# Kernel optimization log

Measured on AMD Instinct MI355X. Metric: run time of the kernel, lower is better.

Reference implementation:

```python
import jax, jax.numpy as jnp
import numpy as np

B, N, C, H = 4, 2048, 768, 12


def setup_inputs() -> dict:
    key = jax.random.key(0)
    k1, k2, k3 = jax.random.split(key, 3)
    x = jax.random.normal(k1, (B, N, C), dtype=jnp.float32)
    qkv_w = jax.random.normal(k2, (3 * C, C), dtype=jnp.float32) * 0.02
    proj_w = jax.random.normal(k3, (C, C), dtype=jnp.float32) * 0.02
    proj_b = jnp.zeros((C,), dtype=jnp.float32)
    return {"x": x, "qkv_w": qkv_w, "proj_w": proj_w, "proj_b": proj_b}


def reference(x, qkv_w, proj_w, proj_b):
    b, n, c = x.shape
    hd = c // H
    scale = hd ** -0.5
    # qkv projection (no bias): (B,N,3C) -> (3,B,H,N,hd)
    qkv = (x @ qkv_w.T).reshape(b, n, 3, H, hd).transpose(2, 0, 3, 1, 4)
    q = qkv[0] * scale
    k = qkv[1]
    v = qkv[2]
    attn = jax.nn.softmax(jnp.einsum('bhqd,bhkd->bhqk', q, k), axis=-1)
    out = jnp.einsum('bhqk,bhkd->bhqd', attn, v)  # (B,H,N,hd)
    out = out.transpose(0, 2, 1, 3).reshape(b, n, c)
    return out @ proj_w.T + proj_b
```

## Files before the change

kernel.cpp:

```cpp
#include <hip/hip_runtime.h>

#define B_SZ 4
#define SEQ  2048
#define CH   768
#define NH   12
#define HD   64

typedef float f32x4  __attribute__((ext_vector_type(4)));
typedef __bf16 bf16x8 __attribute__((ext_vector_type(8)));
typedef __bf16 bf16x2 __attribute__((ext_vector_type(2)));

#define MFMA16(a,b,c) __builtin_amdgcn_mfma_f32_16x16x32_bf16(a,b,c,0,0,0)

#define QSCALE 0.1803368801111204f

#if __has_builtin(__builtin_amdgcn_exp2f)
#define EXP2(x) __builtin_amdgcn_exp2f(x)
#else
#define EXP2(x) exp2f(x)
#endif

#define SWZ(row) (((row) ^ ((row) >> 3)) & 7)

__device__ __forceinline__ unsigned pack2(float a, float b) {
    union { bf16x2 v; unsigned u; } p;
    p.v[0] = (__bf16)a; p.v[1] = (__bf16)b;
    return p.u;
}

__device__ __forceinline__ void lds_dma16(const void* g, void* l) {
    __builtin_amdgcn_global_load_lds(
        (const __attribute__((address_space(1))) void*)g,
        (__attribute__((address_space(3))) void*)(unsigned)(unsigned long long)l,
        16, 0, 0);
}

#define NBLK_X  6144
#define NBLK_W  1728
#define NBLK_P   576
__global__ __launch_bounds__(256) void convert_all(const float* __restrict__ x,
                                                   const float* __restrict__ w,
                                                   const float* __restrict__ p,
                                                   __bf16* __restrict__ ox,
                                                   __bf16* __restrict__ ow,
                                                   __bf16* __restrict__ op) {
    int blk = blockIdx.x;
    const float* src;
    __bf16* dst;
    int base;
    if (blk < NBLK_X)               { src = x; dst = ox; base = blk; }
    else if (blk < NBLK_X + NBLK_W) { src = w; dst = ow; base = blk - NBLK_X; }
    else                            { src = p; dst = op; base = blk - NBLK_X - NBLK_W; }
    int i = (base * 256 + threadIdx.x) * 4;
    float4 v = *(const float4*)(src + i);
    union { __bf16 h[4]; uint2 u; } o;
    o.h[0] = (__bf16)v.x; o.h[1] = (__bf16)v.y; o.h[2] = (__bf16)v.z; o.h[3] = (__bf16)v.w;
    *(uint2*)(dst + i) = o.u;
}

__device__ __forceinline__ void gemm128_loop(const __bf16* __restrict__ A,
                                             const __bf16* __restrict__ Bm,
                                             int K, int rowBlk, int colBlk,
                                             __bf16* As, __bf16* Bs,
                                             f32x4 acc[4][4]) {
    const int tid  = threadIdx.x;
    const int lane = tid & 63, wid = tid >> 6;
    const int quad = lane >> 4, l16 = lane & 15;
    const int wm = wid >> 1, wn = wid & 1;

    f32x4 z = {0.f, 0.f, 0.f, 0.f};
#pragma unroll
    for (int mi = 0; mi < 4; ++mi)
#pragma unroll
        for (int ni = 0; ni < 4; ++ni) acc[mi][ni] = z;

    for (int k0 = 0; k0 < K; k0 += 64) {
        __syncthreads();
#pragma unroll
        for (int i = 0; i < 4; ++i) {
            int s = i * 256 + tid;
            int row = s >> 3, pc = s & 7;
            int lc = pc ^ (row & 7);
            lds_dma16(A  + (size_t)(rowBlk + row) * K + k0 + lc * 8, As + s * 8);
            lds_dma16(Bm + (size_t)(colBlk + row) * K + k0 + lc * 8, Bs + s * 8);
        }
        __syncthreads();

#pragma unroll
        for (int kc = 0; kc < 2; ++kc) {
            bf16x8 af[4], bfr[4];
#pragma unroll
            for (int mi = 0; mi < 4; ++mi) {
                int row = wm * 64 + mi * 16 + l16;
                int pc = (quad + 4 * kc) ^ (row & 7);
                af[mi] = *(const bf16x8*)(As + row * 64 + pc * 8);
            }
#pragma unroll
            for (int ni = 0; ni < 4; ++ni) {
                int row = wn * 64 + ni * 16 + l16;
                int pc = (quad + 4 * kc) ^ (row & 7);
                bfr[ni] = *(const bf16x8*)(Bs + row * 64 + pc * 8);
            }
#pragma unroll
            for (int mi = 0; mi < 4; ++mi)
#pragma unroll
                for (int ni = 0; ni < 4; ++ni)
                    acc[mi][ni] = MFMA16(af[mi], bfr[ni], acc[mi][ni]);
        }
    }
}

__global__ __launch_bounds__(256) void qkv_gemm(const __bf16* __restrict__ Xb,
                                                const __bf16* __restrict__ Wb,
                                                __bf16* __restrict__ Qb,
                                                __bf16* __restrict__ Kb,
                                                __bf16* __restrict__ Vt) {
    __shared__ __bf16 smem[128 * 128];
    f32x4 acc[4][4];
    const int rowBlk = blockIdx.x * 128, colBlk = blockIdx.y * 128;
    gemm128_loop(Xb, Wb, CH, rowBlk, colBlk, smem, smem + 128 * 64, acc);

    const int tid = threadIdx.x;
    const int lane = tid & 63, wid = tid >> 6;
    const int quad = lane >> 4, l16 = lane & 15, wm = wid >> 1, wn = wid & 1;
    const int b = rowBlk >> 11, n0 = rowBlk & (SEQ - 1);

    if (colBlk < 2 * CH) {
        const int isK = (colBlk >= CH);
#pragma unroll
        for (int mi = 0; mi < 4; ++mi)
#pragma unroll
            for (int ni = 0; ni < 4; ++ni)
#pragma unroll
                for (int r = 0; r < 4; ++r) {
                    int n = n0 + wm * 64 + mi * 16 + quad * 4 + r;
                    int cc = colBlk - (isK ? CH : 0) + wn * 64 + ni * 16 + l16;
                    int h = cc >> 6, d = cc & 63;
                    size_t idx = (size_t)((b * NH + h) * SEQ + n) * HD + d;
                    float v = acc[mi][ni][r];
                    if (isK) Kb[idx] = (__bf16)v;
                    else     Qb[idx] = (__bf16)(v * QSCALE);
                }
    } else {
        const int vblk = colBlk - 2 * CH;
        __syncthreads();
#pragma unroll
        for (int mi = 0; mi < 4; ++mi)
#pragma unroll
            for (int ni = 0; ni < 4; ++ni)
#pragma unroll
                for (int r = 0; r < 4; ++r) {
                    int rl = wm * 64 + mi * 16 + quad * 4 + r;
                    int cl = wn * 64 + ni * 16 + l16;
                    smem[cl * 128 + (((rl >> 3) ^ (cl & 15)) << 3) + (rl & 7)] =
                        (__bf16)acc[mi][ni][r];
                }
        __syncthreads();
        const int dl = tid >> 1;
        const int d  = vblk + dl;
        const int h  = d >> 6, dd = d & 63;
        const size_t base = (size_t)((b * NH + h) * HD + dd) * SEQ + n0;
#pragma unroll
        for (int j2 = 0; j2 < 8; ++j2) {
            int j = (tid & 1) * 8 + j2;
            uint4 val = *(const uint4*)(smem + dl * 128 + ((j ^ (dl & 15)) << 3));
            *(uint4*)(Vt + base + j * 8) = val;
        }
    }
}

__global__ __launch_bounds__(256, 3) void flash_attn(const __bf16* __restrict__ Qb,
                                                     const __bf16* __restrict__ Kb,
                                                     const __bf16* __restrict__ Vt,
                                                     __bf16* __restrict__ Ab) {
    __shared__ __bf16 smem[16384];

    const int tid  = threadIdx.x;
    const int lane = tid & 63, wid = tid >> 6;
    const int quad = lane >> 4, l16 = lane & 15;

    const int lin  = blockIdx.x;
    const int xcd  = lin & 7, idx = lin >> 3;
    const int bh   = xcd * 6 + (idx >> 4);
    const int qblk = idx & 15;
    const int b    = bh / NH, head = bh - b * NH;

    const int qA = qblk * 128 + wid * 16 + l16;
    const int qB = qA + 64;

    bf16x8 qfA[2], qfB[2];
#pragma unroll
    for (int kcd = 0; kcd < 2; ++kcd) {
        qfA[kcd] = *(const bf16x8*)(Qb + (size_t)(bh * SEQ + qA) * HD + kcd * 32 + quad * 8);
        qfB[kcd] = *(const bf16x8*)(Qb + (size_t)(bh * SEQ + qB) * HD + kcd * 32 + quad * 8);
    }

    const int key_e = ((l16 >> 2) << 3) + (l16 & 3);
    const int key_o = ((((l16 >> 2) ^ 1)) << 3) + 4 + (l16 & 3);

    f32x4 otA[4], otB[4];
    f32x4 z = {0.f, 0.f, 0.f, 0.f};
#pragma unroll
    for (int dg = 0; dg < 4; ++dg) { otA[dg] = z; otB[dg] = z; }
    float lA = 0.f, lB = 0.f;

    const __bf16* Kbh = Kb + (size_t)bh * SEQ * HD;
    const __bf16* Vbh = Vt + (size_t)bh * HD * SEQ;

    const int s_row = tid >> 3, s_pc = tid & 7;
    const int s_lc0 = s_pc ^ SWZ(s_row);
    const int s_lc1 = s_pc ^ SWZ(s_row + 32);

#define PROCESS(Ks, Vs)                                                                       \
    do {                                                                                      \
        f32x4 stA[4], stB[4];                                                                 \
        _Pragma("unroll")                                                                     \
        for (int g = 0; g < 4; ++g) { stA[g] = z; stB[g] = z; }                               \
        _Pragma("unroll")                                                                     \
        for (int g = 0; g < 4; ++g) {                                                         \
            const int key = ((g >> 1) << 5) + ((g & 1) ? key_o : key_e);                      \
            _Pragma("unroll")                                                                 \
            for (int kcd = 0; kcd < 2; ++kcd) {                                               \
                int c8 = quad + (kcd << 2);                                                   \
                bf16x8 kf = *(const bf16x8*)((Ks) + key * 64 + ((c8 ^ SWZ(key)) << 3));       \
                stA[g] = MFMA16(kf, qfA[kcd], stA[g]);                                        \
                stB[g] = MFMA16(kf, qfB[kcd], stB[g]);                                        \
            }                                                                                 \
        }                                                                                     \
        bf16x8 pfA[2], pfB[2];                                                                \
        _Pragma("unroll")                                                                     \
        for (int g = 0; g < 4; ++g)                                                           \
            _Pragma("unroll")                                                                 \
            for (int r = 0; r < 4; ++r) {                                                     \
                float p = EXP2(stA[g][r]);                                                    \
                stA[g][r] = p;                                                                \
                lA += p;                                                                      \
            }                                                                                 \
        _Pragma("unroll")                                                                     \
        for (int kk = 0; kk < 2; ++kk) {                                                      \
            unsigned w0 = pack2(stA[2 * kk][0], stA[2 * kk][1]);                              \
            unsigned w1 = pack2(stA[2 * kk][2], stA[2 * kk][3]);                              \
            unsigned x0 = pack2(stA[2 * kk + 1][0], stA[2 * kk + 1][1]);                      \
            unsigned x1 = pack2(stA[2 * kk + 1][2], stA[2 * kk + 1][3]);                      \
            unsigned w2 = (unsigned)__shfl_xor((int)x0, 16, 64);                              \
            unsigned w3 = (unsigned)__shfl_xor((int)x1, 16, 64);                              \
            union { bf16x8 v; unsigned u[4]; } f;                                             \
            f.u[0] = w0; f.u[1] = w1; f.u[2] = w2; f.u[3] = w3;                               \
            pfA[kk] = f.v;                                                                    \
        }                                                                                     \
        _Pragma("unroll")                                                                     \
        for (int g = 0; g < 4; ++g)                                                           \
            _Pragma("unroll")                                                                 \
            for (int r = 0; r < 4; ++r) {                                                     \
                float p = EXP2(stB[g][r]);                                                    \
                stB[g][r] = p;                                                                \
                lB += p;                                                                      \
            }                                                                                 \
        _Pragma("unroll")                                                                     \
        for (int kk = 0; kk < 2; ++kk) {                                                      \
            unsigned w0 = pack2(stB[2 * kk][0], stB[2 * kk][1]);                              \
            unsigned w1 = pack2(stB[2 * kk][2], stB[2 * kk][3]);                              \
            unsigned x0 = pack2(stB[2 * kk + 1][0], stB[2 * kk + 1][1]);                      \
            unsigned x1 = pack2(stB[2 * kk + 1][2], stB[2 * kk + 1][3]);                      \
            unsigned w2 = (unsigned)__shfl_xor((int)x0, 16, 64);                              \
            unsigned w3 = (unsigned)__shfl_xor((int)x1, 16, 64);                              \
            union { bf16x8 v; unsigned u[4]; } f;                                             \
            f.u[0] = w0; f.u[1] = w1; f.u[2] = w2; f.u[3] = w3;                               \
            pfB[kk] = f.v;                                                                    \
        }                                                                                     \
        _Pragma("unroll")                                                                     \
        for (int dg = 0; dg < 4; ++dg)                                                        \
            _Pragma("unroll")                                                                 \
            for (int kk = 0; kk < 2; ++kk) {                                                  \
                int row = (dg << 4) + l16;                                                    \
                int c8 = quad + (kk << 2);                                                    \
                bf16x8 vf = *(const bf16x8*)((Vs) + row * 64 + ((c8 ^ SWZ(row)) << 3));       \
                otA[dg] = MFMA16(vf, pfA[kk], otA[dg]);                                       \
                otB[dg] = MFMA16(vf, pfB[kk], otB[dg]);                                       \
            }                                                                                 \
    } while (0)

    for (int kb = 0; kb < SEQ / 128; ++kb) {
        const int kbase = kb * 128;
        __syncthreads();
        lds_dma16(Kbh + (size_t)(kbase + s_row) * HD + s_lc0 * 8,            smem + tid * 8);
        lds_dma16(Kbh + (size_t)(kbase + s_row + 32) * HD + s_lc1 * 8,       smem + 2048 + tid * 8);
        lds_dma16(Vbh + (size_t)s_row * SEQ + kbase + s_lc0 * 8,             smem + 4096 + tid * 8);
        lds_dma16(Vbh + (size_t)(s_row + 32) * SEQ + kbase + s_lc1 * 8,      smem + 6144 + tid * 8);
        lds_dma16(Kbh + (size_t)(kbase + 64 + s_row) * HD + s_lc0 * 8,       smem + 8192 + tid * 8);
        lds_dma16(Kbh + (size_t)(kbase + 96 + s_row) * HD + s_lc1 * 8,       smem + 10240 + tid * 8);
        lds_dma16(Vbh + (size_t)s_row * SEQ + kbase + 64 + s_lc0 * 8,        smem + 12288 + tid * 8);
        lds_dma16(Vbh + (size_t)(s_row + 32) * SEQ + kbase + 64 + s_lc1 * 8, smem + 14336 + tid * 8);
        __syncthreads();

        PROCESS(smem, smem + 4096);
        PROCESS(smem + 8192, smem + 12288);
    }
#undef PROCESS

    lA += __shfl_xor(lA, 16, 64);
    lA += __shfl_xor(lA, 32, 64);
    lB += __shfl_xor(lB, 16, 64);
    lB += __shfl_xor(lB, 32, 64);
    const float rA = 1.f / lA, rB = 1.f / lB;

    __syncthreads();
    __bf16 (*Ob)[72] = (__bf16(*)[72])smem;
#pragma unroll
    for (int dg = 0; dg < 4; ++dg)
#pragma unroll
        for (int r = 0; r < 4; ++r) {
            int d = (dg << 4) + (quad << 2) + r;
            Ob[wid * 16 + l16][d]      = (__bf16)(otA[dg][r] * rA);
            Ob[64 + wid * 16 + l16][d] = (__bf16)(otB[dg][r] * rB);
        }
    __syncthreads();
    {
        const int row = tid >> 1, c0 = (tid & 1) * 32;
        __bf16* dst = Ab + (size_t)(b * SEQ + qblk * 128 + row) * CH + head * HD + c0;
#pragma unroll
        for (int j = 0; j < 4; ++j)
            *(uint4*)(dst + j * 8) = *(const uint4*)(&Ob[row][c0 + j * 8]);
    }
}

__global__ __launch_bounds__(256) void proj_gemm(const __bf16* __restrict__ Ab,
                                                 const __bf16* __restrict__ Pw,
                                                 const float* __restrict__ bias,
                                                 float* __restrict__ out) {
    __shared__ __bf16 As[128 * 64];
    __shared__ __bf16 Bs[128 * 64];
    f32x4 acc[4][4];
    const int rowBlk = blockIdx.x * 128, colBlk = blockIdx.y * 128;
    gemm128_loop(Ab, Pw, CH, rowBlk, colBlk, As, Bs, acc);

    const int lane = threadIdx.x & 63, wid = threadIdx.x >> 6;
    const int quad = lane >> 4, l16 = lane & 15, wm = wid >> 1, wn = wid & 1;
#pragma unroll
    for (int mi = 0; mi < 4; ++mi)
#pragma unroll
        for (int ni = 0; ni < 4; ++ni)
#pragma unroll
            for (int r = 0; r < 4; ++r) {
                int row = rowBlk + wm * 64 + mi * 16 + quad * 4 + r;
                int col = colBlk + wn * 64 + ni * 16 + l16;
                out[(size_t)row * CH + col] = acc[mi][ni][r] + bias[col];
            }
}

extern "C" void kernel_launch(void* const* d_in, const int* in_sizes, int n_in,
                              void* d_out, int out_size, void* d_ws, size_t ws_size,
                              hipStream_t stream) {
    const float* x      = (const float*)d_in[0];
    const float* qkv_w  = (const float*)d_in[1];
    const float* proj_w = (const float*)d_in[2];
    const float* proj_b = (const float*)d_in[3];
    float* out = (float*)d_out;

    char* ws = (char*)d_ws;
    const size_t nX = (size_t)B_SZ * SEQ * CH;
    const size_t nW = (size_t)3 * CH * CH;
    const size_t nP = (size_t)CH * CH;
    const size_t nQ = (size_t)B_SZ * NH * SEQ * HD;

    __bf16* Xb = (__bf16*)(ws);
    __bf16* Wb = (__bf16*)(ws + 2 * nX);
    __bf16* Pw = (__bf16*)(ws + 2 * (nX + nW));
    __bf16* Qb = (__bf16*)(ws + 2 * (nX + nW + nP));
    __bf16* Kb = (__bf16*)(ws + 2 * (nX + nW + nP + nQ));
    __bf16* Vt = (__bf16*)(ws + 2 * (nX + nW + nP + 2 * nQ));
    __bf16* Ab = (__bf16*)(ws + 2 * (nX + nW + nP + 3 * nQ));

    convert_all<<<NBLK_X + NBLK_W + NBLK_P, 256, 0, stream>>>(x, qkv_w, proj_w, Xb, Wb, Pw);

    qkv_gemm<<<dim3((B_SZ * SEQ) / 128, (3 * CH) / 128), 256, 0, stream>>>(Xb, Wb, Qb, Kb, Vt);

    flash_attn<<<768, 256, 0, stream>>>(Qb, Kb, Vt, Ab);

    proj_gemm<<<dim3((B_SZ * SEQ) / 128, CH / 128), 256, 0, stream>>>(Ab, Pw, proj_b, out);
}
```

Measured before the change: 210.4 us.

## Triple-buffer K/V tiles with async LDS DMA prefetch and MFMA priority hints

Replaces the synchronous load-then-compute loop over 128-key blocks with a 64-key triple-buffered LDS pipeline. The next tile is prefetched with LDS DMA while the current one is processed, using a partial vmcnt wait and a single barrier per step. s_setprio is raised around the MFMA sections, and the exp/sum reduction is rewritten as a pairwise tree. LDS use grows from 32KB to 48KB, which may cut occupancy below the 3 blocks/CU launch bound, and the single barrier with three rotating buffers depends on careful ordering to avoid overwriting a buffer still in use.

```diff
diff --git a/kernel.cpp b/kernel.cpp
--- a/kernel.cpp
+++ b/kernel.cpp
@@ -173,7 +173,7 @@
                                                      const __bf16* __restrict__ Kb,
                                                      const __bf16* __restrict__ Vt,
                                                      __bf16* __restrict__ Ab) {
-    __shared__ __bf16 smem[16384];
+    __shared__ __bf16 smem[24576];
 
     const int tid  = threadIdx.x;
     const int lane = tid & 63, wid = tid >> 6;
@@ -211,11 +211,23 @@
     const int s_lc0 = s_pc ^ SWZ(s_row);
     const int s_lc1 = s_pc ^ SWZ(s_row + 32);
 
+#define STAGE(buf, kb_)                                                                        \
+    do {                                                                                       \
+        __bf16* Ks_ = smem + (buf) * 8192;                                                     \
+        __bf16* Vs_ = Ks_ + 4096;                                                              \
+        const int kbase_ = (kb_) * 64;                                                         \
+        lds_dma16(Kbh + (size_t)(kbase_ + s_row) * HD + s_lc0 * 8,       Ks_ + tid * 8);       \
+        lds_dma16(Kbh + (size_t)(kbase_ + s_row + 32) * HD + s_lc1 * 8,  Ks_ + 2048 + tid * 8);\
+        lds_dma16(Vbh + (size_t)s_row * SEQ + kbase_ + s_lc0 * 8,        Vs_ + tid * 8);       \
+        lds_dma16(Vbh + (size_t)(s_row + 32) * SEQ + kbase_ + s_lc1 * 8, Vs_ + 2048 + tid * 8);\
+    } while (0)
+
 #define PROCESS(Ks, Vs)                                                                       \
     do {                                                                                      \
         f32x4 stA[4], stB[4];                                                                 \
         _Pragma("unroll")                                                                     \
         for (int g = 0; g < 4; ++g) { stA[g] = z; stB[g] = z; }                               \
+        __builtin_amdgcn_s_setprio(1);                                                        \
         _Pragma("unroll")                                                                     \
         for (int g = 0; g < 4; ++g) {                                                         \
             const int key = ((g >> 1) << 5) + ((g & 1) ? key_o : key_e);                      \
@@ -227,15 +239,15 @@
                 stB[g] = MFMA16(kf, qfB[kcd], stB[g]);                                        \
             }                                                                                 \
         }                                                                                     \
+        __builtin_amdgcn_s_setprio(0);                                                        \
         bf16x8 pfA[2], pfB[2];                                                                \
         _Pragma("unroll")                                                                     \
-        for (int g = 0; g < 4; ++g)                                                           \
-            _Pragma("unroll")                                                                 \
-            for (int r = 0; r < 4; ++r) {                                                     \
-                float p = EXP2(stA[g][r]);                                                    \
-                stA[g][r] = p;                                                                \
-                lA += p;                                                                      \
-            }                                                                                 \
+        for (int g = 0; g < 4; ++g) {                                                         \
+            float p0 = EXP2(stA[g][0]), p1 = EXP2(stA[g][1]);                                 \
+            float p2 = EXP2(stA[g][2]), p3 = EXP2(stA[g][3]);                                 \
+            stA[g][0] = p0; stA[g][1] = p1; stA[g][2] = p2; stA[g][3] = p3;                   \
+            lA += (p0 + p1) + (p2 + p3);                                                      \
+        }                                                                                     \
         _Pragma("unroll")                                                                     \
         for (int kk = 0; kk < 2; ++kk) {                                                      \
             unsigned w0 = pack2(stA[2 * kk][0], stA[2 * kk][1]);                              \
@@ -249,13 +261,12 @@
             pfA[kk] = f.v;                                                                    \
         }                                                                                     \
         _Pragma("unroll")                                                                     \
-        for (int g = 0; g < 4; ++g)                                                           \
-            _Pragma("unroll")                                                                 \
-            for (int r = 0; r < 4; ++r) {                                                     \
-                float p = EXP2(stB[g][r]);                                                    \
-                stB[g][r] = p;                                                                \
-                lB += p;                                                                      \
-            }                                                                                 \
+        for (int g = 0; g < 4; ++g) {                                                         \
+            float p0 = EXP2(stB[g][0]), p1 = EXP2(stB[g][1]);                                 \
+            float p2 = EXP2(stB[g][2]), p3 = EXP2(stB[g][3]);                                 \
+            stB[g][0] = p0; stB[g][1] = p1; stB[g][2] = p2; stB[g][3] = p3;                   \
+            lB += (p0 + p1) + (p2 + p3);                                                      \
+        }                                                                                     \
         _Pragma("unroll")                                                                     \
         for (int kk = 0; kk < 2; ++kk) {                                                      \
             unsigned w0 = pack2(stB[2 * kk][0], stB[2 * kk][1]);                              \
@@ -268,6 +279,7 @@
             f.u[0] = w0; f.u[1] = w1; f.u[2] = w2; f.u[3] = w3;                               \
             pfB[kk] = f.v;                                                                    \
         }                                                                                     \
+        __builtin_amdgcn_s_setprio(1);                                                        \
         _Pragma("unroll")                                                                     \
         for (int dg = 0; dg < 4; ++dg)                                                        \
             _Pragma("unroll")                                                                 \
@@ -278,25 +290,29 @@
                 otA[dg] = MFMA16(vf, pfA[kk], otA[dg]);                                       \
                 otB[dg] = MFMA16(vf, pfB[kk], otB[dg]);                                       \
             }                                                                                 \
+        __builtin_amdgcn_s_setprio(0);                                                        \
     } while (0)
 
-    for (int kb = 0; kb < SEQ / 128; ++kb) {
-        const int kbase = kb * 128;
-        __syncthreads();
-        lds_dma16(Kbh + (size_t)(kbase + s_row) * HD + s_lc0 * 8,            smem + tid * 8);
-        lds_dma16(Kbh + (size_t)(kbase + s_row + 32) * HD + s_lc1 * 8,       smem + 2048 + tid * 8);
-        lds_dma16(Vbh + (size_t)s_row * SEQ + kbase + s_lc0 * 8,             smem + 4096 + tid * 8);
-        lds_dma16(Vbh + (size_t)(s_row + 32) * SEQ + kbase + s_lc1 * 8,      smem + 6144 + tid * 8);
-        lds_dma16(Kbh + (size_t)(kbase + 64 + s_row) * HD + s_lc0 * 8,       smem + 8192 + tid * 8);
-        lds_dma16(Kbh + (size_t)(kbase + 96 + s_row) * HD + s_lc1 * 8,       smem + 10240 + tid * 8);
-        lds_dma16(Vbh + (size_t)s_row * SEQ + kbase + 64 + s_lc0 * 8,        smem + 12288 + tid * 8);
-        lds_dma16(Vbh + (size_t)(s_row + 32) * SEQ + kbase + 64 + s_lc1 * 8, smem + 14336 + tid * 8);
-        __syncthreads();
-
-        PROCESS(smem, smem + 4096);
-        PROCESS(smem + 8192, smem + 12288);
+    STAGE(0, 0);
+    int cur = 0, nxt = 1;
+#pragma unroll 1
+    for (int t = 0; t < SEQ / 64; ++t) {
+        if (t + 1 < SEQ / 64) {
+            STAGE(nxt, t + 1);
+            asm volatile("s_waitcnt vmcnt(4)" ::: "memory");
+        } else {
+            asm volatile("s_waitcnt vmcnt(0)" ::: "memory");
+        }
+        __builtin_amdgcn_s_barrier();
+        __builtin_amdgcn_sched_barrier(0);
+        const __bf16* Ks = smem + cur * 8192;
+        const __bf16* Vs = Ks + 4096;
+        PROCESS(Ks, Vs);
+        cur = nxt;
+        nxt = (nxt == 2) ? 0 : nxt + 1;
     }
 #undef PROCESS
+#undef STAGE
 
     lA += __shfl_xor(lA, 16, 64);
     lA += __shfl_xor(lA, 32, 64);
```

New measurement: 209.4 us. About the same (-0.5%).

## Double-buffer K tiles in LDS and load V straight into registers

Applied to the files above, without the earlier changes.

The attention main loop now runs over 64-key tiles. The K tile is double-buffered in LDS, so the next tile's DMA is issued before the current tile is consumed, which means one barrier per iteration instead of two. V fragments are loaded directly from global memory into registers instead of being staged in LDS, which cuts the LDS footprint and LDS read traffic. MFMA sections are wrapped in s_setprio to favour matrix issue. The risks are uncoalesced or latency-exposed global V loads and reliance on the barrier to cover the async K DMA.

```diff
diff --git a/kernel.cpp b/kernel.cpp
--- a/kernel.cpp
+++ b/kernel.cpp
@@ -173,7 +173,7 @@
                                                      const __bf16* __restrict__ Kb,
                                                      const __bf16* __restrict__ Vt,
                                                      __bf16* __restrict__ Ab) {
-    __shared__ __bf16 smem[16384];
+    __shared__ __bf16 smem[9216];
 
     const int tid  = threadIdx.x;
     const int lane = tid & 63, wid = tid >> 6;
@@ -211,92 +211,101 @@
     const int s_lc0 = s_pc ^ SWZ(s_row);
     const int s_lc1 = s_pc ^ SWZ(s_row + 32);
 
-#define PROCESS(Ks, Vs)                                                                       \
-    do {                                                                                      \
-        f32x4 stA[4], stB[4];                                                                 \
-        _Pragma("unroll")                                                                     \
-        for (int g = 0; g < 4; ++g) { stA[g] = z; stB[g] = z; }                               \
-        _Pragma("unroll")                                                                     \
-        for (int g = 0; g < 4; ++g) {                                                         \
-            const int key = ((g >> 1) << 5) + ((g & 1) ? key_o : key_e);                      \
-            _Pragma("unroll")                                                                 \
-            for (int kcd = 0; kcd < 2; ++kcd) {                                               \
-                int c8 = quad + (kcd << 2);                                                   \
-                bf16x8 kf = *(const bf16x8*)((Ks) + key * 64 + ((c8 ^ SWZ(key)) << 3));       \
-                stA[g] = MFMA16(kf, qfA[kcd], stA[g]);                                        \
-                stB[g] = MFMA16(kf, qfB[kcd], stB[g]);                                        \
-            }                                                                                 \
-        }                                                                                     \
-        bf16x8 pfA[2], pfB[2];                                                                \
-        _Pragma("unroll")                                                                     \
-        for (int g = 0; g < 4; ++g)                                                           \
-            _Pragma("unroll")                                                                 \
-            for (int r = 0; r < 4; ++r) {                                                     \
-                float p = EXP2(stA[g][r]);                                                    \
-                stA[g][r] = p;                                                                \
-                lA += p;                                                                      \
-            }                                                                                 \
-        _Pragma("unroll")                                                                     \
-        for (int kk = 0; kk < 2; ++kk) {                                                      \
-            unsigned w0 = pack2(stA[2 * kk][0], stA[2 * kk][1]);                              \
-            unsigned w1 = pack2(stA[2 * kk][2], stA[2 * kk][3]);                              \
-            unsigned x0 = pack2(stA[2 * kk + 1][0], stA[2 * kk + 1][1]);                      \
-            unsigned x1 = pack2(stA[2 * kk + 1][2], stA[2 * kk + 1][3]);                      \
-            unsigned w2 = (unsigned)__shfl_xor((int)x0, 16, 64);                              \
-            unsigned w3 = (unsigned)__shfl_xor((int)x1, 16, 64);                              \
-            union { bf16x8 v; unsigned u[4]; } f;                                             \
-            f.u[0] = w0; f.u[1] = w1; f.u[2] = w2; f.u[3] = w3;                               \
-            pfA[kk] = f.v;                                                                    \
-        }                                                                                     \
-        _Pragma("unroll")                                                                     \
-        for (int g = 0; g < 4; ++g)                                                           \
-            _Pragma("unroll")                                                                 \
-            for (int r = 0; r < 4; ++r) {                                                     \
-                float p = EXP2(stB[g][r]);                                                    \
-                stB[g][r] = p;                                                                \
-                lB += p;                                                                      \
-            }                                                                                 \
-        _Pragma("unroll")                                                                     \
-        for (int kk = 0; kk < 2; ++kk) {                                                      \
-            unsigned w0 = pack2(stB[2 * kk][0], stB[2 * kk][1]);                              \
-            unsigned w1 = pack2(stB[2 * kk][2], stB[2 * kk][3]);                              \
-            unsigned x0 = pack2(stB[2 * kk + 1][0], stB[2 * kk + 1][1]);                      \
-            unsigned x1 = pack2(stB[2 * kk + 1][2], stB[2 * kk + 1][3]);                      \
-            unsigned w2 = (unsigned)__shfl_xor((int)x0, 16, 64);                              \
-            unsigned w3 = (unsigned)__shfl_xor((int)x1, 16, 64);                              \
-            union { bf16x8 v; unsigned u[4]; } f;                                             \
-            f.u[0] = w0; f.u[1] = w1; f.u[2] = w2; f.u[3] = w3;                               \
-            pfB[kk] = f.v;                                                                    \
-        }                                                                                     \
-        _Pragma("unroll")                                                                     \
-        for (int dg = 0; dg < 4; ++dg)                                                        \
-            _Pragma("unroll")                                                                 \
-            for (int kk = 0; kk < 2; ++kk) {                                                  \
-                int row = (dg << 4) + l16;                                                    \
-                int c8 = quad + (kk << 2);                                                    \
-                bf16x8 vf = *(const bf16x8*)((Vs) + row * 64 + ((c8 ^ SWZ(row)) << 3));       \
-                otA[dg] = MFMA16(vf, pfA[kk], otA[dg]);                                       \
-                otB[dg] = MFMA16(vf, pfB[kk], otB[dg]);                                       \
-            }                                                                                 \
+#define STAGE_K(buf, kb_)                                                                      \
+    do {                                                                                       \
+        __bf16* Ks_ = smem + (buf) * 4096;                                                     \
+        const int kbase_ = (kb_) * 64;                                                         \
+        lds_dma16(Kbh + (size_t)(kbase_ + s_row) * HD + s_lc0 * 8,      Ks_ + tid * 8);        \
+        lds_dma16(Kbh + (size_t)(kbase_ + s_row + 32) * HD + s_lc1 * 8, Ks_ + 2048 + tid * 8); \
     } while (0)
 
-    for (int kb = 0; kb < SEQ / 128; ++kb) {
-        const int kbase = kb * 128;
-        __syncthreads();
-        lds_dma16(Kbh + (size_t)(kbase + s_row) * HD + s_lc0 * 8,            smem + tid * 8);
-        lds_dma16(Kbh + (size_t)(kbase + s_row + 32) * HD + s_lc1 * 8,       smem + 2048 + tid * 8);
-        lds_dma16(Vbh + (size_t)s_row * SEQ + kbase + s_lc0 * 8,             smem + 4096 + tid * 8);
-        lds_dma16(Vbh + (size_t)(s_row + 32) * SEQ + kbase + s_lc1 * 8,      smem + 6144 + tid * 8);
-        lds_dma16(Kbh + (size_t)(kbase + 64 + s_row) * HD + s_lc0 * 8,       smem + 8192 + tid * 8);
-        lds_dma16(Kbh + (size_t)(kbase + 96 + s_row) * HD + s_lc1 * 8,       smem + 10240 + tid * 8);
-        lds_dma16(Vbh + (size_t)s_row * SEQ + kbase + 64 + s_lc0 * 8,        smem + 12288 + tid * 8);
-        lds_dma16(Vbh + (size_t)(s_row + 32) * SEQ + kbase + 64 + s_lc1 * 8, smem + 14336 + tid * 8);
-        __syncthreads();
-
-        PROCESS(smem, smem + 4096);
-        PROCESS(smem + 8192, smem + 12288);
-    }
-#undef PROCESS
+    STAGE_K(0, 0);
+
+#pragma unroll 1
+    for (int t = 0; t < SEQ / 64; ++t) {
+        const int kbase = t * 64;
+        __syncthreads();
+
+        bf16x8 vr[8];
+#pragma unroll
+        for (int dg = 0; dg < 4; ++dg)
+#pragma unroll
+            for (int kk = 0; kk < 2; ++kk)
+                vr[dg * 2 + kk] = *(const bf16x8*)(Vbh + (size_t)(dg * 16 + l16) * SEQ
+                                                   + kbase + ((quad + 4 * kk) << 3));
+
+        if (t + 1 < SEQ / 64) STAGE_K((t + 1) & 1, t + 1);
+
+        const __bf16* Ks = smem + (t & 1) * 4096;
+
+        f32x4 stA[4], stB[4];
+#pragma unroll
+        for (int g = 0; g < 4; ++g) { stA[g] = z; stB[g] = z; }
+        __builtin_amdgcn_s_setprio(1);
+#pragma unroll
+        for (int g = 0; g < 4; ++g) {
+            const int key = ((g >> 1) << 5) + ((g & 1) ? key_o : key_e);
+#pragma unroll
+            for (int kcd = 0; kcd < 2; ++kcd) {
+                int c8 = quad + (kcd << 2);
+                bf16x8 kf = *(const bf16x8*)(Ks + key * 64 + ((c8 ^ SWZ(key)) << 3));
+                stA[g] = MFMA16(kf, qfA[kcd], stA[g]);
+                stB[g] = MFMA16(kf, qfB[kcd], stB[g]);
+            }
+        }
+        __builtin_amdgcn_s_setprio(0);
+
+        bf16x8 pfA[2], pfB[2];
+#pragma unroll
+        for (int g = 0; g < 4; ++g) {
+            float p0 = EXP2(stA[g][0]), p1 = EXP2(stA[g][1]);
+            float p2 = EXP2(stA[g][2]), p3 = EXP2(stA[g][3]);
+            stA[g][0] = p0; stA[g][1] = p1; stA[g][2] = p2; stA[g][3] = p3;
+            lA += (p0 + p1) + (p2 + p3);
+        }
+#pragma unroll
+        for (int kk = 0; kk < 2; ++kk) {
+            unsigned w0 = pack2(stA[2 * kk][0], stA[2 * kk][1]);
+            unsigned w1 = pack2(stA[2 * kk][2], stA[2 * kk][3]);
+            unsigned x0 = pack2(stA[2 * kk + 1][0], stA[2 * kk + 1][1]);
+            unsigned x1 = pack2(stA[2 * kk + 1][2], stA[2 * kk + 1][3]);
+            unsigned w2 = (unsigned)__shfl_xor((int)x0, 16, 64);
+            unsigned w3 = (unsigned)__shfl_xor((int)x1, 16, 64);
+            union { bf16x8 v; unsigned u[4]; } f;
+            f.u[0] = w0; f.u[1] = w1; f.u[2] = w2; f.u[3] = w3;
+            pfA[kk] = f.v;
+        }
+#pragma unroll
+        for (int g = 0; g < 4; ++g) {
+            float p0 = EXP2(stB[g][0]), p1 = EXP2(stB[g][1]);
+            float p2 = EXP2(stB[g][2]), p3 = EXP2(stB[g][3]);
+            stB[g][0] = p0; stB[g][1] = p1; stB[g][2] = p2; stB[g][3] = p3;
+            lB += (p0 + p1) + (p2 + p3);
+        }
+#pragma unroll
+        for (int kk = 0; kk < 2; ++kk) {
+            unsigned w0 = pack2(stB[2 * kk][0], stB[2 * kk][1]);
+            unsigned w1 = pack2(stB[2 * kk][2], stB[2 * kk][3]);
+            unsigned x0 = pack2(stB[2 * kk + 1][0], stB[2 * kk + 1][1]);
+            unsigned x1 = pack2(stB[2 * kk + 1][2], stB[2 * kk + 1][3]);
+            unsigned w2 = (unsigned)__shfl_xor((int)x0, 16, 64);
+            unsigned w3 = (unsigned)__shfl_xor((int)x1, 16, 64);
+            union { bf16x8 v; unsigned u[4]; } f;
+            f.u[0] = w0; f.u[1] = w1; f.u[2] = w2; f.u[3] = w3;
+            pfB[kk] = f.v;
+        }
+
+        __builtin_amdgcn_s_setprio(1);
+#pragma unroll
+        for (int dg = 0; dg < 4; ++dg)
+#pragma unroll
+            for (int kk = 0; kk < 2; ++kk) {
+                otA[dg] = MFMA16(vr[dg * 2 + kk], pfA[kk], otA[dg]);
+                otB[dg] = MFMA16(vr[dg * 2 + kk], pfB[kk], otB[dg]);
+            }
+        __builtin_amdgcn_s_setprio(0);
+    }
+#undef STAGE_K
 
     lA += __shfl_xor(lA, 16, 64);
     lA += __shfl_xor(lA, 32, 64);
```

Result: slower. 253.8 us (+20.6%).

## Split attention work per wave across query-halves and key-halves with LDS reduction

Applied to the files above, without the earlier changes.

Reassigns the four waves so each handles 64 queries (four 16-row groups) over half of each 64-key chunk, rather than 32 queries over all keys. Each K and V fragment read from LDS now feeds four MFMAs instead of two, which cuts LDS read traffic per MFMA. The cost is two partial outputs per query that must be merged at the end through an fp32 LDS scratch buffer, which raises shared memory to about 52KB. It also raises accumulator register pressure (16 output tiles per wave), which may reduce occupancy below the launch-bounds target of 3 blocks.

```diff
diff --git a/kernel.cpp b/kernel.cpp
--- a/kernel.cpp
+++ b/kernel.cpp
@@ -173,11 +173,13 @@
                                                      const __bf16* __restrict__ Kb,
                                                      const __bf16* __restrict__ Vt,
                                                      __bf16* __restrict__ Ab) {
-    __shared__ __bf16 smem[16384];
+    __shared__ __bf16 smem[26112];
 
     const int tid  = threadIdx.x;
     const int lane = tid & 63, wid = tid >> 6;
     const int quad = lane >> 4, l16 = lane & 15;
+    const int qh = wid & 1;
+    const int kh = wid >> 1;
 
     const int lin  = blockIdx.x;
     const int xcd  = lin & 7, idx = lin >> 3;
@@ -185,24 +187,28 @@
     const int qblk = idx & 15;
     const int b    = bh / NH, head = bh - b * NH;
 
-    const int qA = qblk * 128 + wid * 16 + l16;
-    const int qB = qA + 64;
-
-    bf16x8 qfA[2], qfB[2];
-#pragma unroll
-    for (int kcd = 0; kcd < 2; ++kcd) {
-        qfA[kcd] = *(const bf16x8*)(Qb + (size_t)(bh * SEQ + qA) * HD + kcd * 32 + quad * 8);
-        qfB[kcd] = *(const bf16x8*)(Qb + (size_t)(bh * SEQ + qB) * HD + kcd * 32 + quad * 8);
+    bf16x8 qf[4][2];
+#pragma unroll
+    for (int qg = 0; qg < 4; ++qg) {
+        const int q = qblk * 128 + qh * 64 + qg * 16 + l16;
+#pragma unroll
+        for (int kcd = 0; kcd < 2; ++kcd)
+            qf[qg][kcd] = *(const bf16x8*)(Qb + (size_t)(bh * SEQ + q) * HD + kcd * 32 + quad * 8);
     }
 
     const int key_e = ((l16 >> 2) << 3) + (l16 & 3);
     const int key_o = ((((l16 >> 2) ^ 1)) << 3) + 4 + (l16 & 3);
-
-    f32x4 otA[4], otB[4];
+    const int key0 = (kh << 5) + key_e;
+    const int key1 = (kh << 5) + key_o;
+    const int swz_k0 = SWZ(key0), swz_k1 = SWZ(key1);
+
+    f32x4 ot[4][4];
     f32x4 z = {0.f, 0.f, 0.f, 0.f};
 #pragma unroll
-    for (int dg = 0; dg < 4; ++dg) { otA[dg] = z; otB[dg] = z; }
-    float lA = 0.f, lB = 0.f;
+    for (int qg = 0; qg < 4; ++qg)
+#pragma unroll
+        for (int dg = 0; dg < 4; ++dg) ot[qg][dg] = z;
+    float l[4] = {0.f, 0.f, 0.f, 0.f};
 
     const __bf16* Kbh = Kb + (size_t)bh * SEQ * HD;
     const __bf16* Vbh = Vt + (size_t)bh * HD * SEQ;
@@ -211,73 +217,47 @@
     const int s_lc0 = s_pc ^ SWZ(s_row);
     const int s_lc1 = s_pc ^ SWZ(s_row + 32);
 
-#define PROCESS(Ks, Vs)                                                                       \
+#define PROCESS(KsP, VsP)                                                                     \
     do {                                                                                      \
-        f32x4 stA[4], stB[4];                                                                 \
+        f32x4 st[4][2];                                                                       \
         _Pragma("unroll")                                                                     \
-        for (int g = 0; g < 4; ++g) { stA[g] = z; stB[g] = z; }                               \
+        for (int qg = 0; qg < 4; ++qg) { st[qg][0] = z; st[qg][1] = z; }                      \
         _Pragma("unroll")                                                                     \
-        for (int g = 0; g < 4; ++g) {                                                         \
-            const int key = ((g >> 1) << 5) + ((g & 1) ? key_o : key_e);                      \
+        for (int kcd = 0; kcd < 2; ++kcd) {                                                   \
+            const int c8 = quad + (kcd << 2);                                                 \
+            bf16x8 kf0 = *(const bf16x8*)((KsP) + key0 * 64 + ((c8 ^ swz_k0) << 3));          \
+            bf16x8 kf1 = *(const bf16x8*)((KsP) + key1 * 64 + ((c8 ^ swz_k1) << 3));          \
             _Pragma("unroll")                                                                 \
-            for (int kcd = 0; kcd < 2; ++kcd) {                                               \
-                int c8 = quad + (kcd << 2);                                                   \
-                bf16x8 kf = *(const bf16x8*)((Ks) + key * 64 + ((c8 ^ SWZ(key)) << 3));       \
-                stA[g] = MFMA16(kf, qfA[kcd], stA[g]);                                        \
-                stB[g] = MFMA16(kf, qfB[kcd], stB[g]);                                        \
+            for (int qg = 0; qg < 4; ++qg) {                                                  \
+                st[qg][0] = MFMA16(kf0, qf[qg][kcd], st[qg][0]);                              \
+                st[qg][1] = MFMA16(kf1, qf[qg][kcd], st[qg][1]);                              \
             }                                                                                 \
         }                                                                                     \
-        bf16x8 pfA[2], pfB[2];                                                                \
+        bf16x8 pf[4];                                                                         \
         _Pragma("unroll")                                                                     \
-        for (int g = 0; g < 4; ++g)                                                           \
-            _Pragma("unroll")                                                                 \
-            for (int r = 0; r < 4; ++r) {                                                     \
-                float p = EXP2(stA[g][r]);                                                    \
-                stA[g][r] = p;                                                                \
-                lA += p;                                                                      \
-            }                                                                                 \
-        _Pragma("unroll")                                                                     \
-        for (int kk = 0; kk < 2; ++kk) {                                                      \
-            unsigned w0 = pack2(stA[2 * kk][0], stA[2 * kk][1]);                              \
-            unsigned w1 = pack2(stA[2 * kk][2], stA[2 * kk][3]);                              \
-            unsigned x0 = pack2(stA[2 * kk + 1][0], stA[2 * kk + 1][1]);                      \
-            unsigned x1 = pack2(stA[2 * kk + 1][2], stA[2 * kk + 1][3]);                      \
+        for (int qg = 0; qg < 4; ++qg) {                                                      \
+            float p0 = EXP2(st[qg][0][0]), p1 = EXP2(st[qg][0][1]);                           \
+            float p2 = EXP2(st[qg][0][2]), p3 = EXP2(st[qg][0][3]);                           \
+            float p4 = EXP2(st[qg][1][0]), p5 = EXP2(st[qg][1][1]);                           \
+            float p6 = EXP2(st[qg][1][2]), p7 = EXP2(st[qg][1][3]);                           \
+            l[qg] += (p0 + p1) + (p2 + p3) + (p4 + p5) + (p6 + p7);                           \
+            unsigned w0 = pack2(p0, p1), w1 = pack2(p2, p3);                                  \
+            unsigned x0 = pack2(p4, p5), x1 = pack2(p6, p7);                                  \
             unsigned w2 = (unsigned)__shfl_xor((int)x0, 16, 64);                              \
             unsigned w3 = (unsigned)__shfl_xor((int)x1, 16, 64);                              \
             union { bf16x8 v; unsigned u[4]; } f;                                             \
             f.u[0] = w0; f.u[1] = w1; f.u[2] = w2; f.u[3] = w3;                               \
-            pfA[kk] = f.v;                                                                    \
+            pf[qg] = f.v;                                                                     \
         }                                                                                     \
         _Pragma("unroll")                                                                     \
-        for (int g = 0; g < 4; ++g)                                                           \
+        for (int dg = 0; dg < 4; ++dg) {                                                      \
+            const int vrow = (dg << 4) + l16;                                                 \
+            bf16x8 vf = *(const bf16x8*)((VsP) + vrow * 64 +                                  \
+                                         (((quad + (kh << 2)) ^ SWZ(vrow)) << 3));            \
             _Pragma("unroll")                                                                 \
-            for (int r = 0; r < 4; ++r) {                                                     \
-                float p = EXP2(stB[g][r]);                                                    \
-                stB[g][r] = p;                                                                \
-                lB += p;                                                                      \
-            }                                                                                 \
-        _Pragma("unroll")                                                                     \
-        for (int kk = 0; kk < 2; ++kk) {                                                      \
-            unsigned w0 = pack2(stB[2 * kk][0], stB[2 * kk][1]);                              \
-            unsigned w1 = pack2(stB[2 * kk][2], stB[2 * kk][3]);                              \
-            unsigned x0 = pack2(stB[2 * kk + 1][0], stB[2 * kk + 1][1]);                      \
-            unsigned x1 = pack2(stB[2 * kk + 1][2], stB[2 * kk + 1][3]);                      \
-            unsigned w2 = (unsigned)__shfl_xor((int)x0, 16, 64);                              \
-            unsigned w3 = (unsigned)__shfl_xor((int)x1, 16, 64);                              \
-            union { bf16x8 v; unsigned u[4]; } f;                                             \
-            f.u[0] = w0; f.u[1] = w1; f.u[2] = w2; f.u[3] = w3;                               \
-            pfB[kk] = f.v;                                                                    \
+            for (int qg = 0; qg < 4; ++qg)                                                    \
+                ot[qg][dg] = MFMA16(vf, pf[qg], ot[qg][dg]);                                  \
         }                                                                                     \
-        _Pragma("unroll")                                                                     \
-        for (int dg = 0; dg < 4; ++dg)                                                        \
-            _Pragma("unroll")                                                                 \
-            for (int kk = 0; kk < 2; ++kk) {                                                  \
-                int row = (dg << 4) + l16;                                                    \
-                int c8 = quad + (kk << 2);                                                    \
-                bf16x8 vf = *(const bf16x8*)((Vs) + row * 64 + ((c8 ^ SWZ(row)) << 3));       \
-                otA[dg] = MFMA16(vf, pfA[kk], otA[dg]);                                       \
-                otB[dg] = MFMA16(vf, pfB[kk], otB[dg]);                                       \
-            }                                                                                 \
     } while (0)
 
     for (int kb = 0; kb < SEQ / 128; ++kb) {
@@ -298,22 +278,42 @@
     }
 #undef PROCESS
 
-    lA += __shfl_xor(lA, 16, 64);
-    lA += __shfl_xor(lA, 32, 64);
-    lB += __shfl_xor(lB, 16, 64);
-    lB += __shfl_xor(lB, 32, 64);
-    const float rA = 1.f / lA, rB = 1.f / lB;
+#pragma unroll
+    for (int qg = 0; qg < 4; ++qg) {
+        l[qg] += __shfl_xor(l[qg], 16, 64);
+        l[qg] += __shfl_xor(l[qg], 32, 64);
+    }
 
     __syncthreads();
-    __bf16 (*Ob)[72] = (__bf16(*)[72])smem;
-#pragma unroll
-    for (int dg = 0; dg < 4; ++dg)
-#pragma unroll
-        for (int r = 0; r < 4; ++r) {
-            int d = (dg << 4) + (quad << 2) + r;
-            Ob[wid * 16 + l16][d]      = (__bf16)(otA[dg][r] * rA);
-            Ob[64 + wid * 16 + l16][d] = (__bf16)(otB[dg][r] * rB);
-        }
+    float* Sc  = (float*)smem;
+    float* Lsc = (float*)(smem + 25600);
+    __bf16 (*Ob)[72] = (__bf16(*)[72])(smem + 16384);
+
+    if (kh == 1) {
+#pragma unroll
+        for (int qg = 0; qg < 4; ++qg) {
+            const int qrow = (qh << 6) + (qg << 4) + l16;
+#pragma unroll
+            for (int dg = 0; dg < 4; ++dg)
+                *(f32x4*)(Sc + qrow * 64 + (dg << 4) + (quad << 2)) = ot[qg][dg];
+            if (quad == 0) Lsc[qrow] = l[qg];
+        }
+    }
+    __syncthreads();
+    if (kh == 0) {
+#pragma unroll
+        for (int qg = 0; qg < 4; ++qg) {
+            const int qrow = (qh << 6) + (qg << 4) + l16;
+            const float r = 1.f / (l[qg] + Lsc[qrow]);
+#pragma unroll
+            for (int dg = 0; dg < 4; ++dg) {
+                f32x4 o = ot[qg][dg] + *(const f32x4*)(Sc + qrow * 64 + (dg << 4) + (quad << 2));
+#pragma unroll
+                for (int rr = 0; rr < 4; ++rr)
+                    Ob[qrow][(dg << 4) + (quad << 2) + rr] = (__bf16)(o[rr] * r);
+            }
+        }
+    }
     __syncthreads();
     {
         const int row = tid >> 1, c0 = (tid & 1) * 32;
```

Measured after the change: 319.2 us. 51.7% more time.
